# Performance work log

Hardware: AMD Instinct MI355X
Metric: run time of the kernel (lower is better)

## Reference

```python
import jax, jax.numpy as jnp
import numpy as np
import math

D_MODEL = 1024
N_HEADS = 16
B, T = 4, 2048


def setup_inputs() -> dict:
    key = jax.random.key(0)
    ks = jax.random.split(key, 10)
    s = 1.0 / math.sqrt(D_MODEL)
    x = jax.random.normal(ks[0], (B, T, D_MODEL), dtype=jnp.float32)
    # causal mask, broadcastable over batch and heads; 0 -> masked
    mask = jnp.tril(jnp.ones((T, T), dtype=jnp.int32))[None, None, :, :]
    w_q = jax.random.normal(ks[1], (D_MODEL, D_MODEL), dtype=jnp.float32) * s
    b_q = jnp.zeros((D_MODEL,), dtype=jnp.float32)
    w_k = jax.random.normal(ks[2], (D_MODEL, D_MODEL), dtype=jnp.float32) * s
    b_k = jnp.zeros((D_MODEL,), dtype=jnp.float32)
    w_v = jax.random.normal(ks[3], (D_MODEL, D_MODEL), dtype=jnp.float32) * s
    b_v = jnp.zeros((D_MODEL,), dtype=jnp.float32)
    w_o = jax.random.normal(ks[4], (D_MODEL, D_MODEL), dtype=jnp.float32) * s
    b_o = jnp.zeros((D_MODEL,), dtype=jnp.float32)
    return {"x": x, "mask": mask, "w_q": w_q, "b_q": b_q, "w_k": w_k,
            "b_k": b_k, "w_v": w_v, "b_v": b_v, "w_o": w_o, "b_o": b_o}


def reference(x, mask, w_q, b_q, w_k, b_k, w_v, b_v, w_o, b_o):
    Bx, Tx, C = x.shape
    H = N_HEADS
    d_k = C // H
    def split_heads(y):  # [B,T,C] -> [B,H,T,d_k]
        return y.reshape(Bx, Tx, H, d_k).transpose(0, 2, 1, 3)
    Q = split_heads(x @ w_q + b_q)
    K = split_heads(x @ w_k + b_k)
    V = split_heads(x @ w_v + b_v)
    scores = jnp.einsum('bhqd,bhkd->bhqk', Q, K) / math.sqrt(d_k)
    scores = jnp.where(mask == 0, jnp.float32(-1e9), scores)
    attn = jax.nn.softmax(scores, axis=-1)
    out = jnp.einsum('bhqk,bhkd->bhqd', attn, V)
    out = out.transpose(0, 2, 1, 3).reshape(Bx, Tx, C)
    return out @ w_o + b_o
```

## Files before the change

### kernel.cpp

```cpp
#include <hip/hip_runtime.h>
#include <stdint.h>

#define D_MODEL 1024
#define NH      16
#define BB      4
#define TT      2048
#define MROWS   (BB * TT)

typedef __attribute__((ext_vector_type(8))) short bf16x8;
typedef __attribute__((ext_vector_type(4))) short bf16x4;
typedef __attribute__((ext_vector_type(4))) float f32x4;

__device__ __forceinline__ unsigned short f2bf(float f) {
    union { float f; unsigned int u; } v; v.f = f;
    unsigned int r = v.u + 0x7fffu + ((v.u >> 16) & 1u);
    return (unsigned short)(r >> 16);
}

__device__ __forceinline__ unsigned short f2bf_fast(float f) {
    union { float f; unsigned int u; } v; v.f = f;
    return (unsigned short)((v.u + 0x8000u) >> 16);
}

__device__ __forceinline__ f32x4 mfma_16x16x16_bf16(bf16x4 a, bf16x4 b, f32x4 c) {
    asm("v_mfma_f32_16x16x16_bf16 %0, %1, %2, %0" : "+v"(c) : "v"(a), "v"(b));
    return c;
}

__device__ __forceinline__ void gload_lds16(const unsigned short* g, unsigned short* l) {
    __builtin_amdgcn_global_load_lds(
        (const __attribute__((address_space(1))) void*)g,
        (__attribute__((address_space(3))) void*)l,
        16, 0, 0);
}

__global__ void prep_kernel(const float* __restrict__ x, unsigned short* __restrict__ xb,
                            const float* __restrict__ wq, const float* __restrict__ wk,
                            const float* __restrict__ wv, const float* __restrict__ wo,
                            unsigned short* tq, unsigned short* tk,
                            unsigned short* tv, unsigned short* to_) {
    if (blockIdx.z == 4) {
        int base = (blockIdx.y * 32 + blockIdx.x) * 2048 + threadIdx.x;
        #pragma unroll
        for (int j = 0; j < 8; ++j) {
            int i = base + j * 256;
            float4 v = ((const float4*)x)[i];
            ushort4 o;
            o.x = f2bf(v.x); o.y = f2bf(v.y); o.z = f2bf(v.z); o.w = f2bf(v.w);
            ((ushort4*)xb)[i] = o;
        }
        return;
    }
    const float* src; unsigned short* dst;
    switch (blockIdx.z) {
        case 0:  src = wq; dst = tq; break;
        case 1:  src = wk; dst = tk; break;
        case 2:  src = wv; dst = tv; break;
        default: src = wo; dst = to_; break;
    }
    __shared__ float tile[32][33];
    int tx = threadIdx.x & 31, ty = threadIdx.x >> 5;
    int k0 = blockIdx.y * 32, n0 = blockIdx.x * 32;
    #pragma unroll
    for (int i = 0; i < 4; ++i)
        tile[ty + i * 8][tx] = src[(k0 + ty + i * 8) * D_MODEL + n0 + tx];
    __syncthreads();
    #pragma unroll
    for (int i = 0; i < 4; ++i)
        dst[(n0 + ty + i * 8) * D_MODEL + k0 + tx] = f2bf(tile[tx][ty + i * 8]);
}

__device__ __forceinline__ void gemm_mainloop(const unsigned short* __restrict__ A,
                                              const unsigned short* __restrict__ Bt,
                                              int m0, int n0,
                                              unsigned short* As, unsigned short* Bs,
                                              f32x4 acc[4][4]) {
    const int tid = threadIdx.x;
    const int lane = tid & 63, wave = tid >> 6;
    const int wm = (wave >> 1) * 64, wn = (wave & 1) * 64;
    const int l15 = lane & 15, quad = lane >> 4;
    const int rx7 = l15 & 7;
    const int srow = tid >> 3;
    const int scol = ((tid & 7) ^ (srow & 7)) * 8;
    const unsigned short* Ag = A + (size_t)(m0 + srow) * D_MODEL + scol;
    const unsigned short* Bg = Bt + (size_t)(n0 + srow) * D_MODEL + scol;
    unsigned short* AsW = As + wave * 512;
    unsigned short* BsW = Bs + wave * 512;
    for (int k0 = 0; k0 < D_MODEL; k0 += 64) {
        __syncthreads();
        #pragma unroll
        for (int p = 0; p < 4; ++p) {
            gload_lds16(Ag + k0 + (size_t)(32 * p) * D_MODEL, AsW + (32 * p) * 64);
            gload_lds16(Bg + k0 + (size_t)(32 * p) * D_MODEL, BsW + (32 * p) * 64);
        }
        __syncthreads();
        #pragma unroll
        for (int kk = 0; kk < 2; ++kk) {
            const int co = ((kk * 4 + quad) ^ rx7) * 8;
            bf16x8 af[4], bfr[4];
            #pragma unroll
            for (int mt = 0; mt < 4; ++mt)
                af[mt] = *(const bf16x8*)(As + (wm + mt * 16 + l15) * 64 + co);
            #pragma unroll
            for (int nt = 0; nt < 4; ++nt)
                bfr[nt] = *(const bf16x8*)(Bs + (wn + nt * 16 + l15) * 64 + co);
            #pragma unroll
            for (int mt = 0; mt < 4; ++mt)
                #pragma unroll
                for (int nt = 0; nt < 4; ++nt)
                    acc[mt][nt] = __builtin_amdgcn_mfma_f32_16x16x32_bf16(af[mt], bfr[nt], acc[mt][nt], 0, 0, 0);
        }
    }
}

__global__ __launch_bounds__(256, 2) void gemm_qkv_kernel(
        const unsigned short* __restrict__ Xb, const unsigned short* __restrict__ Wt,
        const float* __restrict__ bq, const float* __restrict__ bk, const float* __restrict__ bv,
        unsigned short* __restrict__ Qo, unsigned short* __restrict__ Ko,
        unsigned short* __restrict__ VTo) {
    __shared__ unsigned short S[18432];
    unsigned short* As = S;
    unsigned short* Bs = S + 8192;
    int m0 = blockIdx.y * 128, n0 = blockIdx.x * 128;
    f32x4 acc[4][4];
    #pragma unroll
    for (int mt = 0; mt < 4; ++mt)
        #pragma unroll
        for (int nt = 0; nt < 4; ++nt)
            acc[mt][nt] = (f32x4){0.f, 0.f, 0.f, 0.f};
    gemm_mainloop(Xb, Wt, m0, n0, As, Bs, acc);

    const int sel = n0 >> 10;
    const float* bias = (sel == 0) ? bq : (sel == 1) ? bk : bv;
    const float scale = (sel == 0) ? 0.125f * 1.44269504f : 1.f;
    const int tid = threadIdx.x, lane = tid & 63, wave = tid >> 6;
    const int wm = (wave >> 1) * 64, wn = (wave & 1) * 64, l15 = lane & 15, quad = lane >> 4;
    if (sel < 2) {
        unsigned short* Out = (sel == 0) ? Qo : Ko;
        __syncthreads();
        unsigned short* R = S + (wn >> 6) * 9216;
        #pragma unroll
        for (int nt = 0; nt < 4; ++nt) {
            int ln = nt * 16 + l15;
            int col = (n0 + wn + nt * 16 + l15) & 1023;
            float bv_ = bias[col];
            #pragma unroll
            for (int mt = 0; mt < 4; ++mt)
                #pragma unroll
                for (int r = 0; r < 4; ++r) {
                    int lm = wm + mt * 16 + quad * 4 + r;
                    R[lm * 72 + ln] = f2bf((acc[mt][nt][r] + bv_) * scale);
                }
        }
        __syncthreads();
        int hh = tid >> 7, t = tid & 127;
        int h0 = (n0 & 1023) >> 6;
        int b = m0 >> 11, tb = m0 & 2047;
        unsigned short* gp = Out + (size_t)((b * NH + h0 + hh) * TT + tb + t) * 64;
        const unsigned short* lp = S + hh * 9216 + t * 72;
        #pragma unroll
        for (int j = 0; j < 8; ++j)
            *(uint4*)(gp + j * 8) = *(const uint4*)(lp + j * 8);
    } else {
        #pragma unroll
        for (int nt = 0; nt < 4; ++nt) {
            int col = (n0 + wn + nt * 16 + l15) & 1023;
            float bv_ = bias[col];
            int h = col >> 6, dd = col & 63;
            #pragma unroll
            for (int mt = 0; mt < 4; ++mt) {
                int gm0 = m0 + wm + mt * 16 + quad * 4;
                int b = gm0 >> 11, t0 = gm0 & 2047;
                ushort4 o;
                o.x = f2bf(acc[mt][nt][0] + bv_);
                o.y = f2bf(acc[mt][nt][1] + bv_);
                o.z = f2bf(acc[mt][nt][2] + bv_);
                o.w = f2bf(acc[mt][nt][3] + bv_);
                *(ushort4*)&VTo[(((size_t)(b * NH + h) * 16 + (t0 >> 7)) * 64 + dd) * 128 + (t0 & 127)] = o;
            }
        }
    }
}

__global__ __launch_bounds__(256, 2) void gemm_out_kernel(
        const unsigned short* __restrict__ Ob, const unsigned short* __restrict__ Wto,
        const float* __restrict__ bo, float* __restrict__ out) {
    __shared__ unsigned short As[128 * 64], Bs[128 * 64];
    int m0 = blockIdx.y * 128, n0 = blockIdx.x * 128;
    f32x4 acc[4][4];
    #pragma unroll
    for (int mt = 0; mt < 4; ++mt)
        #pragma unroll
        for (int nt = 0; nt < 4; ++nt)
            acc[mt][nt] = (f32x4){0.f, 0.f, 0.f, 0.f};
    gemm_mainloop(Ob, Wto, m0, n0, As, Bs, acc);
    const int tid = threadIdx.x, lane = tid & 63, wave = tid >> 6;
    const int wm = (wave >> 1) * 64, wn = (wave & 1) * 64, l15 = lane & 15, quad = lane >> 4;
    #pragma unroll
    for (int nt = 0; nt < 4; ++nt) {
        int gn = n0 + wn + nt * 16 + l15;
        float bv_ = bo[gn];
        #pragma unroll
        for (int mt = 0; mt < 4; ++mt) {
            #pragma unroll
            for (int r = 0; r < 4; ++r) {
                int gm = m0 + wm + mt * 16 + quad * 4 + r;
                out[(size_t)gm * D_MODEL + gn] = acc[mt][nt][r] + bv_;
            }
        }
    }
}

__global__ __launch_bounds__(512, 4) void flash_kernel(
        const unsigned short* __restrict__ Q, const unsigned short* __restrict__ K,
        const unsigned short* __restrict__ VT, unsigned short* __restrict__ O) {
    __shared__ unsigned short S[18432];
    unsigned short* Kd = S;
    unsigned short* Vd = S + 8192;
    const int n = blockIdx.x;
    const int bh = n & 63;
    const int pr = n >> 6;
    const int tid = threadIdx.x, lane = tid & 63, wave = tid >> 6;
    const int g = wave >> 2;
    const int qt = g ? pr : (15 - pr);
    const int q0 = qt * 128;
    const int l15 = lane & 15, quad = lane >> 4;
    const int mbase = (wave & 3) * 32;
    const unsigned short* Qb = Q + (size_t)bh * (TT * 64) + (size_t)q0 * 64;
    const unsigned short* Kb = K + (size_t)bh * (TT * 64);
    const unsigned short* Vtb = VT + (size_t)bh * (16 * 8192);

    const int kr = tid >> 3, ks = tid & 7;
    const int koff = kr * 64 + ((ks ^ (kr & 7)) * 8);
    const int voff = kr * 128 + ((ks ^ (kr & 7)) * 8);
    auto fire = [&](int kt, int buf) {
        gload_lds16(Kb + kt * 4096 + koff, Kd + buf * 4096 + wave * 512);
        gload_lds16(Vtb + (kt >> 1) * 8192 + (kt & 1) * 64 + voff, Vd + buf * 4096 + wave * 512);
    };

    bf16x8 qf[2][2];
    #pragma unroll
    for (int mt = 0; mt < 2; ++mt)
        #pragma unroll
        for (int kk = 0; kk < 2; ++kk)
            qf[mt][kk] = *(const bf16x8*)(Qb + (size_t)(mbase + mt * 16 + l15) * 64 + kk * 32 + quad * 8);

    bf16x4 ones;
    ones[0] = ones[1] = ones[2] = ones[3] = (short)0x3F80;
    f32x4 acc_l[2];
    f32x4 acc[2][4];
    #pragma unroll
    for (int mt = 0; mt < 2; ++mt) {
        acc_l[mt] = (f32x4){0.f, 0.f, 0.f, 0.f};
        #pragma unroll
        for (int nt = 0; nt < 4; ++nt) acc[mt][nt] = (f32x4){0.f, 0.f, 0.f, 0.f};
    }

    fire(0, 0);

    const int nkt = 32 - 2 * pr;
    for (int kt = 0; kt < nkt; ++kt) {
        const int p = kt & 1;
        __syncthreads();
        if (kt + 1 < nkt) fire(kt + 1, p ^ 1);
        if (kt * 64 > q0 + mbase + 31) continue;
        const unsigned short* Ksl = Kd + p * 4096;
        const unsigned short* Vsl = Vd + p * 4096;

        f32x4 sf[2][2][2];
        #pragma unroll
        for (int s4 = 0; s4 < 2; ++s4)
            #pragma unroll
            for (int mt = 0; mt < 2; ++mt)
                #pragma unroll
                for (int ntl = 0; ntl < 2; ++ntl) sf[s4][mt][ntl] = (f32x4){0.f, 0.f, 0.f, 0.f};
        __builtin_amdgcn_s_setprio(1);
        #pragma unroll
        for (int s4 = 0; s4 < 2; ++s4)
            #pragma unroll
            for (int kk = 0; kk < 2; ++kk)
                #pragma unroll
                for (int ntl = 0; ntl < 2; ++ntl) {
                    int row = s4 * 32 + ntl * 16 + l15;
                    bf16x8 kf = *(const bf16x8*)&Ksl[row * 64 + (((kk * 4 + quad) ^ (row & 7)) * 8)];
                    #pragma unroll
                    for (int mt = 0; mt < 2; ++mt)
                        sf[s4][mt][ntl] = __builtin_amdgcn_mfma_f32_16x16x32_bf16(kf, qf[mt][kk], sf[s4][mt][ntl], 0, 0, 0);
                }
        __builtin_amdgcn_s_setprio(0);
        if (kt >= 2 * qt) {
            const int kofs = (kt - 2 * qt) * 64;
            #pragma unroll
            for (int s4 = 0; s4 < 2; ++s4)
                #pragma unroll
                for (int mt = 0; mt < 2; ++mt) {
                    int qi = mbase + mt * 16 + l15;
                    #pragma unroll
                    for (int ntl = 0; ntl < 2; ++ntl)
                        #pragma unroll
                        for (int r = 0; r < 4; ++r) {
                            int ki = kofs + s4 * 32 + ntl * 16 + quad * 4 + r;
                            if (ki > qi) sf[s4][mt][ntl][r] = -1e30f;
                        }
                }
        }
        bf16x4 pa[2][2][2];
        #pragma unroll
        for (int s4 = 0; s4 < 2; ++s4) {
            #pragma unroll
            for (int mt = 0; mt < 2; ++mt)
                #pragma unroll
                for (int ntl = 0; ntl < 2; ++ntl) {
                    bf16x4 pk;
                    pk[0] = (short)f2bf_fast(__builtin_amdgcn_exp2f(sf[s4][mt][ntl][0]));
                    pk[1] = (short)f2bf_fast(__builtin_amdgcn_exp2f(sf[s4][mt][ntl][1]));
                    pk[2] = (short)f2bf_fast(__builtin_amdgcn_exp2f(sf[s4][mt][ntl][2]));
                    pk[3] = (short)f2bf_fast(__builtin_amdgcn_exp2f(sf[s4][mt][ntl][3]));
                    pa[s4][mt][ntl] = pk;
                }
            __builtin_amdgcn_s_setprio(1);
            #pragma unroll
            for (int ntl = 0; ntl < 2; ++ntl) {
                #pragma unroll
                for (int ntv = 0; ntv < 4; ++ntv) {
                    int d = ntv * 16 + l15;
                    int cch = s4 * 4 + ntl * 2 + (quad >> 1);
                    bf16x4 vf = *(const bf16x4*)&Vsl[d * 64 + ((cch ^ (d & 7)) * 8) + (quad & 1) * 4];
                    #pragma unroll
                    for (int mt = 0; mt < 2; ++mt)
                        acc[mt][ntv] = mfma_16x16x16_bf16(pa[s4][mt][ntl], vf, acc[mt][ntv]);
                }
                #pragma unroll
                for (int mt = 0; mt < 2; ++mt)
                    acc_l[mt] = mfma_16x16x16_bf16(pa[s4][mt][ntl], ones, acc_l[mt]);
            }
            __builtin_amdgcn_s_setprio(0);
        }
    }

    const int b = bh >> 4, h = bh & 15;
    float inv[2][4];
    #pragma unroll
    for (int mt = 0; mt < 2; ++mt)
        #pragma unroll
        for (int r = 0; r < 4; ++r)
            inv[mt][r] = __builtin_amdgcn_rcpf(acc_l[mt][r]);
    __syncthreads();
    unsigned short* Ost = S + g * 9216;
    #pragma unroll
    for (int mt = 0; mt < 2; ++mt)
        #pragma unroll
        for (int nt = 0; nt < 4; ++nt)
            #pragma unroll
            for (int r = 0; r < 4; ++r)
                Ost[(mbase + mt * 16 + quad * 4 + r) * 72 + nt * 16 + l15] =
                    f2bf(acc[mt][nt][r] * inv[mt][r]);
    __syncthreads();
    {
        int row = tid >> 1, seg = tid & 1;
        int gg = row >> 7, r128 = row & 127;
        int qtw = gg ? pr : (15 - pr);
        unsigned short* gp = O + (size_t)(b * TT + qtw * 128 + r128) * D_MODEL + h * 64 + seg * 32;
        const unsigned short* lp = S + gg * 9216 + r128 * 72 + seg * 32;
        #pragma unroll
        for (int j = 0; j < 4; ++j)
            *(uint4*)(gp + j * 8) = *(const uint4*)(lp + j * 8);
    }
}

extern "C" void kernel_launch(void* const* d_in, const int* in_sizes, int n_in,
                              void* d_out, int out_size, void* d_ws, size_t ws_size,
                              hipStream_t stream) {
    const float* x  = (const float*)d_in[0];
    const float* wq = (const float*)d_in[2];
    const float* bq = (const float*)d_in[3];
    const float* wk = (const float*)d_in[4];
    const float* bk = (const float*)d_in[5];
    const float* wv = (const float*)d_in[6];
    const float* bv = (const float*)d_in[7];
    const float* wo = (const float*)d_in[8];
    const float* bo = (const float*)d_in[9];

    char* ws = (char*)d_ws;
    unsigned short* Xb  = (unsigned short*)ws;
    unsigned short* Wtq = (unsigned short*)(ws + (size_t)(16 << 20));
    unsigned short* Wtk = Wtq + (size_t)D_MODEL * D_MODEL;
    unsigned short* Wtv = Wtk + (size_t)D_MODEL * D_MODEL;
    unsigned short* Wto = Wtv + (size_t)D_MODEL * D_MODEL;
    unsigned short* Qb  = Wto + (size_t)D_MODEL * D_MODEL;
    unsigned short* Kb  = Qb + (size_t)MROWS * D_MODEL;
    unsigned short* VTb = Kb + (size_t)MROWS * D_MODEL;
    unsigned short* Ob  = Xb;

    prep_kernel<<<dim3(32, 32, 5), 256, 0, stream>>>(x, Xb, wq, wk, wv, wo, Wtq, Wtk, Wtv, Wto);
    gemm_qkv_kernel<<<dim3(3 * D_MODEL / 128, MROWS / 128), 256, 0, stream>>>(
        Xb, Wtq, bq, bk, bv, Qb, Kb, VTb);
    flash_kernel<<<dim3(8 * 64), 512, 0, stream>>>(Qb, Kb, VTb, Ob);
    gemm_out_kernel<<<dim3(D_MODEL / 128, MROWS / 128), 256, 0, stream>>>(Ob, Wto, bo, (float*)d_out);
}
```

Before: 247.6 us.

## Double-buffer GEMM mainloop LDS with two-stage global-to-LDS prefetch

Converts the shared GEMM mainloop used by the QKV and output projections into a two-deep pipeline. Tiles t+1 and t+2 are loaded directly into LDS while tile t is consumed, and partial vmcnt waits replace the full load-then-sync pattern. This hides global load latency behind MFMA work. In exchange, LDS per block doubles to 64 KB, which may reduce how many blocks fit per CU. Correctness relies on the hand-counted vmcnt values.

Measured after the change: 246.7 us. Within noise of the previous version (-0.4%).

```diff
diff --git a/kernel.cpp b/kernel.cpp
--- a/kernel.cpp
+++ b/kernel.cpp
@@ -73,7 +73,7 @@
 __device__ __forceinline__ void gemm_mainloop(const unsigned short* __restrict__ A,
                                               const unsigned short* __restrict__ Bt,
                                               int m0, int n0,
-                                              unsigned short* As, unsigned short* Bs,
+                                              unsigned short* S,
                                               f32x4 acc[4][4]) {
     const int tid = threadIdx.x;
     const int lane = tid & 63, wave = tid >> 6;
@@ -84,16 +84,27 @@
     const int scol = ((tid & 7) ^ (srow & 7)) * 8;
     const unsigned short* Ag = A + (size_t)(m0 + srow) * D_MODEL + scol;
     const unsigned short* Bg = Bt + (size_t)(n0 + srow) * D_MODEL + scol;
-    unsigned short* AsW = As + wave * 512;
-    unsigned short* BsW = Bs + wave * 512;
-    for (int k0 = 0; k0 < D_MODEL; k0 += 64) {
-        __syncthreads();
+
+    auto stage = [&](int t, int buf) {
+        unsigned short* AsW = S + buf * 16384 + wave * 512;
+        unsigned short* BsW = S + buf * 16384 + 8192 + wave * 512;
+        const int k0 = t * 64;
         #pragma unroll
         for (int p = 0; p < 4; ++p) {
             gload_lds16(Ag + k0 + (size_t)(32 * p) * D_MODEL, AsW + (32 * p) * 64);
             gload_lds16(Bg + k0 + (size_t)(32 * p) * D_MODEL, BsW + (32 * p) * 64);
         }
-        __syncthreads();
+    };
+
+    stage(0, 0);
+    stage(1, 1);
+    for (int t = 0; t < 16; ++t) {
+        if (t < 15) asm volatile("s_waitcnt vmcnt(8)" ::: "memory");
+        else        asm volatile("s_waitcnt vmcnt(0)" ::: "memory");
+        __builtin_amdgcn_s_barrier();
+        asm volatile("" ::: "memory");
+        const unsigned short* As = S + (t & 1) * 16384;
+        const unsigned short* Bs = As + 8192;
         #pragma unroll
         for (int kk = 0; kk < 2; ++kk) {
             const int co = ((kk * 4 + quad) ^ rx7) * 8;
@@ -110,6 +121,9 @@
                 for (int nt = 0; nt < 4; ++nt)
                     acc[mt][nt] = __builtin_amdgcn_mfma_f32_16x16x32_bf16(af[mt], bfr[nt], acc[mt][nt], 0, 0, 0);
         }
+        asm volatile("" ::: "memory");
+        __builtin_amdgcn_s_barrier();
+        if (t + 2 < 16) stage(t + 2, t & 1);
     }
 }
 
@@ -118,9 +132,7 @@
         const float* __restrict__ bq, const float* __restrict__ bk, const float* __restrict__ bv,
         unsigned short* __restrict__ Qo, unsigned short* __restrict__ Ko,
         unsigned short* __restrict__ VTo) {
-    __shared__ unsigned short S[18432];
-    unsigned short* As = S;
-    unsigned short* Bs = S + 8192;
+    __shared__ unsigned short S[32768];
     int m0 = blockIdx.y * 128, n0 = blockIdx.x * 128;
     f32x4 acc[4][4];
     #pragma unroll
@@ -128,7 +140,7 @@
         #pragma unroll
         for (int nt = 0; nt < 4; ++nt)
             acc[mt][nt] = (f32x4){0.f, 0.f, 0.f, 0.f};
-    gemm_mainloop(Xb, Wt, m0, n0, As, Bs, acc);
+    gemm_mainloop(Xb, Wt, m0, n0, S, acc);
 
     const int sel = n0 >> 10;
     const float* bias = (sel == 0) ? bq : (sel == 1) ? bk : bv;
@@ -185,7 +197,7 @@
 __global__ __launch_bounds__(256, 2) void gemm_out_kernel(
         const unsigned short* __restrict__ Ob, const unsigned short* __restrict__ Wto,
         const float* __restrict__ bo, float* __restrict__ out) {
-    __shared__ unsigned short As[128 * 64], Bs[128 * 64];
+    __shared__ unsigned short S[32768];
     int m0 = blockIdx.y * 128, n0 = blockIdx.x * 128;
     f32x4 acc[4][4];
     #pragma unroll
@@ -193,7 +205,7 @@
         #pragma unroll
         for (int nt = 0; nt < 4; ++nt)
             acc[mt][nt] = (f32x4){0.f, 0.f, 0.f, 0.f};
-    gemm_mainloop(Ob, Wto, m0, n0, As, Bs, acc);
+    gemm_mainloop(Ob, Wto, m0, n0, S, acc);
     const int tid = threadIdx.x, lane = tid & 63, wave = tid >> 6;
     const int wm = (wave >> 1) * 64, wn = (wave & 1) * 64, l15 = lane & 15, quad = lane >> 4;
     #pragma unroll
```

## Enlarge QKV GEMM tile to 256x256 with 512 threads and double-buffered LDS

Applied to the files above, without the earlier changes.

The QKV projection GEMM moves from 128x128 tiles with 256 threads to 256x256 tiles with 512 threads (8 waves, each computing 128x64). The main loop is rewritten with an inline double-buffered direct global-to-LDS load pipeline, and wave priority is raised during the MFMA phase. The Q/K epilogue is staged in two halves through LDS. The larger tiles cut global and L2 traffic per FLOP, but they drop the grid to 384 blocks, which may underfill the CUs and adds register and LDS pressure (128KB of shared memory per block).

After: 264.8 us. 1.07x slower.

```diff
diff --git a/kernel.cpp b/kernel.cpp
--- a/kernel.cpp
+++ b/kernel.cpp
@@ -113,64 +113,118 @@
     }
 }
 
-__global__ __launch_bounds__(256, 2) void gemm_qkv_kernel(
+__global__ __launch_bounds__(512, 2) void gemm_qkv_kernel(
         const unsigned short* __restrict__ Xb, const unsigned short* __restrict__ Wt,
         const float* __restrict__ bq, const float* __restrict__ bk, const float* __restrict__ bv,
         unsigned short* __restrict__ Qo, unsigned short* __restrict__ Ko,
         unsigned short* __restrict__ VTo) {
-    __shared__ unsigned short S[18432];
-    unsigned short* As = S;
-    unsigned short* Bs = S + 8192;
-    int m0 = blockIdx.y * 128, n0 = blockIdx.x * 128;
-    f32x4 acc[4][4];
-    #pragma unroll
-    for (int mt = 0; mt < 4; ++mt)
+    __shared__ unsigned short S[65536];
+    const int m0 = blockIdx.y * 256, n0 = blockIdx.x * 256;
+    const int tid = threadIdx.x, lane = tid & 63, wave = tid >> 6;
+    const int l15 = lane & 15, quad = lane >> 4, rx7 = l15 & 7;
+    const int wmRow = (wave >> 2) * 128, wnRow = (wave & 3) * 64;
+
+    const int srow8 = tid >> 3;
+    const int scol = ((tid & 7) ^ (srow8 & 7)) * 8;
+    const unsigned short* Ag = Xb + (size_t)(m0 + srow8) * 1024 + scol;
+    const unsigned short* Bg = Wt + (size_t)(n0 + srow8) * 1024 + scol;
+
+    f32x4 acc[8][4];
+    #pragma unroll
+    for (int mt = 0; mt < 8; ++mt)
         #pragma unroll
         for (int nt = 0; nt < 4; ++nt)
             acc[mt][nt] = (f32x4){0.f, 0.f, 0.f, 0.f};
-    gemm_mainloop(Xb, Wt, m0, n0, As, Bs, acc);
+
+    auto stage = [&](int t, int buf) {
+        unsigned short* Ad = S + buf * 32768 + wave * 512;
+        unsigned short* Bd = S + buf * 32768 + 16384 + wave * 512;
+        const int k0 = t * 64;
+        #pragma unroll
+        for (int p = 0; p < 4; ++p) {
+            gload_lds16(Ag + (size_t)p * 65536 + k0, Ad + p * 4096);
+            gload_lds16(Bg + (size_t)p * 65536 + k0, Bd + p * 4096);
+        }
+    };
+
+    stage(0, 0);
+    asm volatile("s_waitcnt vmcnt(0)" ::: "memory");
+    __builtin_amdgcn_s_barrier();
+    asm volatile("" ::: "memory");
+    for (int t = 0; t < 16; ++t) {
+        const int cur = t & 1;
+        if (t + 1 < 16) stage(t + 1, cur ^ 1);
+        const unsigned short* As = S + cur * 32768;
+        const unsigned short* Bs = As + 16384;
+        __builtin_amdgcn_s_setprio(1);
+        #pragma unroll
+        for (int kk = 0; kk < 2; ++kk) {
+            const int co = ((kk * 4 + quad) ^ rx7) * 8;
+            bf16x8 bfr[4];
+            #pragma unroll
+            for (int nt = 0; nt < 4; ++nt)
+                bfr[nt] = *(const bf16x8*)(Bs + (wnRow + nt * 16 + l15) * 64 + co);
+            #pragma unroll
+            for (int mt = 0; mt < 8; ++mt) {
+                bf16x8 af = *(const bf16x8*)(As + (wmRow + mt * 16 + l15) * 64 + co);
+                #pragma unroll
+                for (int nt = 0; nt < 4; ++nt)
+                    acc[mt][nt] = __builtin_amdgcn_mfma_f32_16x16x32_bf16(af, bfr[nt], acc[mt][nt], 0, 0, 0);
+            }
+        }
+        __builtin_amdgcn_s_setprio(0);
+        asm volatile("" ::: "memory");
+        asm volatile("s_waitcnt vmcnt(0)" ::: "memory");
+        __builtin_amdgcn_s_barrier();
+        asm volatile("" ::: "memory");
+    }
 
     const int sel = n0 >> 10;
     const float* bias = (sel == 0) ? bq : (sel == 1) ? bk : bv;
     const float scale = (sel == 0) ? 0.125f * 1.44269504f : 1.f;
-    const int tid = threadIdx.x, lane = tid & 63, wave = tid >> 6;
-    const int wm = (wave >> 1) * 64, wn = (wave & 1) * 64, l15 = lane & 15, quad = lane >> 4;
+    const int b = m0 >> 11, tb = m0 & 2047;
+    const int nb = n0 & 1023;
     if (sel < 2) {
         unsigned short* Out = (sel == 0) ? Qo : Ko;
-        __syncthreads();
-        unsigned short* R = S + (wn >> 6) * 9216;
+        const int h0 = nb >> 6;
+        const int wq = wave & 3;
+        const int myhalf = wave >> 2;
+        #pragma unroll
+        for (int wh = 0; wh < 2; ++wh) {
+            if (myhalf == wh) {
+                unsigned short* R = S + wq * 9216;
+                #pragma unroll
+                for (int nt = 0; nt < 4; ++nt) {
+                    float bv_ = bias[nb + wq * 64 + nt * 16 + l15];
+                    #pragma unroll
+                    for (int mt = 0; mt < 8; ++mt)
+                        #pragma unroll
+                        for (int r = 0; r < 4; ++r)
+                            R[(mt * 16 + quad * 4 + r) * 72 + nt * 16 + l15] =
+                                f2bf((acc[mt][nt][r] + bv_) * scale);
+                }
+            }
+            __syncthreads();
+            {
+                int hh = tid >> 7, trow = tid & 127;
+                unsigned short* gp = Out + (size_t)((b * NH + h0 + hh) * TT + tb + wh * 128 + trow) * 64;
+                const unsigned short* lp = S + hh * 9216 + trow * 72;
+                #pragma unroll
+                for (int j = 0; j < 8; ++j)
+                    *(uint4*)(gp + j * 8) = *(const uint4*)(lp + j * 8);
+            }
+            __syncthreads();
+        }
+    } else {
         #pragma unroll
         for (int nt = 0; nt < 4; ++nt) {
-            int ln = nt * 16 + l15;
-            int col = (n0 + wn + nt * 16 + l15) & 1023;
-            float bv_ = bias[col];
-            #pragma unroll
-            for (int mt = 0; mt < 4; ++mt)
-                #pragma unroll
-                for (int r = 0; r < 4; ++r) {
-                    int lm = wm + mt * 16 + quad * 4 + r;
-                    R[lm * 72 + ln] = f2bf((acc[mt][nt][r] + bv_) * scale);
-                }
-        }
-        __syncthreads();
-        int hh = tid >> 7, t = tid & 127;
-        int h0 = (n0 & 1023) >> 6;
-        int b = m0 >> 11, tb = m0 & 2047;
-        unsigned short* gp = Out + (size_t)((b * NH + h0 + hh) * TT + tb + t) * 64;
-        const unsigned short* lp = S + hh * 9216 + t * 72;
-        #pragma unroll
-        for (int j = 0; j < 8; ++j)
-            *(uint4*)(gp + j * 8) = *(const uint4*)(lp + j * 8);
-    } else {
-        #pragma unroll
-        for (int nt = 0; nt < 4; ++nt) {
-            int col = (n0 + wn + nt * 16 + l15) & 1023;
-            float bv_ = bias[col];
-            int h = col >> 6, dd = col & 63;
-            #pragma unroll
-            for (int mt = 0; mt < 4; ++mt) {
-                int gm0 = m0 + wm + mt * 16 + quad * 4;
-                int b = gm0 >> 11, t0 = gm0 & 2047;
+            int cc = nb + (wave & 3) * 64 + nt * 16 + l15;
+            float bv_ = bias[cc];
+            int h = cc >> 6, dd = cc & 63;
+            #pragma unroll
+            for (int mt = 0; mt < 8; ++mt) {
+                int gm0 = m0 + (wave >> 2) * 128 + mt * 16 + quad * 4;
+                int t0 = gm0 & 2047;
                 ushort4 o;
                 o.x = f2bf(acc[mt][nt][0] + bv_);
                 o.y = f2bf(acc[mt][nt][1] + bv_);
@@ -393,7 +447,7 @@
     unsigned short* Ob  = Xb;
 
     prep_kernel<<<dim3(32, 32, 5), 256, 0, stream>>>(x, Xb, wq, wk, wv, wo, Wtq, Wtk, Wtv, Wto);
-    gemm_qkv_kernel<<<dim3(3 * D_MODEL / 128, MROWS / 128), 256, 0, stream>>>(
+    gemm_qkv_kernel<<<dim3(12, 32), 512, 0, stream>>>(
         Xb, Wtq, bq, bk, bv, Qb, Kb, VTb);
     flash_kernel<<<dim3(8 * 64), 512, 0, stream>>>(Qb, Kb, VTb, Ob);
     gemm_out_kernel<<<dim3(D_MODEL / 128, MROWS / 128), 256, 0, stream>>>(Ob, Wto, bo, (float*)d_out);
```
